# Performance work log

Hardware: AMD Instinct MI355X
Metric: run time of the kernel (lower is better)

The kernel has to match this reference:

```python
import jax, jax.numpy as jnp
import numpy as np

K_CLS, M_PROTO, C = 19, 10, 720
EPS_SK, SK_ITERS = 0.05, 3  # standard distributed_sinkhorn defaults (SwAV/ProtoSeg)


def _layernorm(x, g, b, eps=1e-5):
    mu = jnp.mean(x, axis=-1, keepdims=True)
    var = jnp.var(x, axis=-1, keepdims=True)
    return (x - mu) * jax.lax.rsqrt(var + eps) * g + b


def _l2n(x):
    return x / jnp.clip(jnp.linalg.norm(x, axis=-1, keepdims=True), 1e-12, None)


def _masked_sinkhorn(scores, mask):
    # scores: [K, N, M] per-class similarity; mask: [K, N] (1.0 where gt_seg == class k)
    # Faithful to distributed_sinkhorn(init_q) run per class, vectorized over classes
    # with masking instead of data-dependent boolean gather (jit-safe).
    L = jnp.exp(scores / EPS_SK) * mask[..., None]                     # [K, N, M]
    L = L / jnp.clip(jnp.sum(L, axis=(1, 2), keepdims=True), 1e-12, None)
    n = jnp.sum(mask, axis=1)[:, None, None]                           # pixels per class [K,1,1]
    n_safe = jnp.maximum(n, 1.0)

    def body(L, _):
        # normalize each prototype row (sum over pixels), then divide by M
        L = L / jnp.clip(jnp.sum(L, axis=1, keepdims=True), 1e-12, None) / M_PROTO
        # normalize each pixel column (sum over prototypes), then divide by n
        L = L / jnp.clip(jnp.sum(L, axis=2, keepdims=True), 1e-12, None) / n_safe
        L = L * mask[..., None]
        return L, None

    L, _ = jax.lax.scan(body, L, None, length=SK_ITERS)
    return L * n_safe                                                  # [K, N, M]


def setup_inputs() -> dict:
    key = jax.random.key(0)
    k1, k2, k3 = jax.random.split(key, 3)
    N = 4 * 128 * 128  # batch 4, 512x512 crop at HRNet output stride 4
    return {
        "x": jax.random.normal(k1, (N, C), jnp.float32),
        "gt_seg": jax.random.randint(k2, (N,), 0, K_CLS),
        "feat_gamma": jnp.ones((C,), jnp.float32),
        "feat_beta": jnp.zeros((C,), jnp.float32),
        "prototypes": jax.random.normal(k3, (K_CLS, M_PROTO, C), jnp.float32) * 0.02,
    }


def reference(x, gt_seg, feat_gamma, feat_beta, prototypes):
    # similarity_compute (cosine branch)
    xn = _l2n(_layernorm(x, feat_gamma, feat_beta))                    # [N, C]
    protos = _l2n(prototypes)                                          # [K, M, C]
    sim_mat = jnp.einsum('nd,kmd->nmk', xn, protos)                    # [N, M, K]

    # prototype_learning
    s = jnp.max(sim_mat, axis=1)                                       # amax over prototypes -> [N, K]
    pred_seg = jnp.argmax(s, axis=-1)                                  # [N]
    scores = jnp.transpose(sim_mat, (2, 0, 1))                         # [K, N, M]
    mask = jnp.transpose(jax.nn.one_hot(gt_seg, K_CLS, dtype=sim_mat.dtype))  # [K, N]
    q = _masked_sinkhorn(scores, mask)                                 # [K, N, M]
    return sim_mat, q, pred_seg
```

## Files before the change

### kernel.cpp

```cpp
#include <hip/hip_runtime.h>
#include <stdint.h>

#define N_PIX    65536
#define C_DIM    720
#define K_CLS    19
#define M_PROTO  10
#define NPROTO   190
#define CPAD     768
#define OFF_Q    12451840
#define OFF_PRED 24903680

typedef _Float16 half8 __attribute__((ext_vector_type(8)));
typedef _Float16 h4    __attribute__((ext_vector_type(4)));
typedef float    f32x4 __attribute__((ext_vector_type(4)));

#define WS_E       0u
#define WS_G2      768u
#define WS_G3      1536u
#define WS_CNT     2304u
#define WS_TIECNT  2432u
#define WS_PSCALE  4096u
#define WS_EPIX    1052672u
#define WS_U       3674112u
#define WS_TIELIST 3936256u
#define WS_PF16    4198400u
#define WS_PF32    4493312u

__device__ __forceinline__ void async16(const void* g, void* l) {
    __builtin_amdgcn_global_load_lds(
        (const __attribute__((address_space(1))) unsigned int*)g,
        (__attribute__((address_space(3))) unsigned int*)l, 16, 0, 0);
}

__global__ void proto_prep(const float* __restrict__ protos,
                           _Float16* __restrict__ pf16,
                           float* __restrict__ pf32,
                           float* __restrict__ wsf) {
    int p = blockIdx.x;
    int tid = threadIdx.x;
    if (p >= NPROTO) {
        for (int c = tid; c < CPAD; c += 256) pf16[(size_t)p * CPAD + c] = (_Float16)0.f;
        if (p == 191) for (int i = tid; i < 640; i += 256) wsf[i] = 0.f;
        return;
    }
    __shared__ float red[256];
    const float* row = protos + (size_t)p * C_DIM;
    float ss = 0.f;
    for (int c = tid; c < C_DIM; c += 256) { float v = row[c]; ss += v * v; }
    red[tid] = ss;
    __syncthreads();
    for (int s = 128; s > 0; s >>= 1) {
        if (tid < s) red[tid] += red[tid + s];
        __syncthreads();
    }
    float invn = 1.f / fmaxf(sqrtf(red[0]), 1e-12f);
    int e8 = p & 7;
    for (int c = tid; c < CPAD; c += 256) {
        float v = (c < C_DIM) ? row[c] * invn : 0.f;
        int sw = (((c >> 3) ^ e8) << 3) | (c & 7);
        pf16[(size_t)p * CPAD + sw] = (_Float16)v;
        if (c < C_DIM) pf32[(size_t)p * C_DIM + c] = v;
    }
}

__global__ __launch_bounds__(256) void gemm_fused(
        const float*  __restrict__ x,
        const float*  __restrict__ gamma,
        const float*  __restrict__ beta,
        const _Float16* __restrict__ pf16,
        const int*    __restrict__ gt_seg,
        float4* __restrict__ pscale,
        float* __restrict__ out_sim,
        float* __restrict__ out_pred,
        float* __restrict__ epix,
        float* __restrict__ E,
        float* __restrict__ cnt,
        int*   __restrict__ tiecnt,
        int*   __restrict__ tielist) {
    extern __shared__ __align__(16) char smem[];
    _Float16* xt = (_Float16*)smem;
    _Float16* ps = (_Float16*)(smem + 49152);

    int tid = threadIdx.x;
    int wave = tid >> 6, lane = tid & 63;
    int lane15 = lane & 15, quad = lane >> 4;
    int n0 = blockIdx.x * 32;
    int ph = wave & 1, qh = wave >> 1;
    int rsub = lane >> 3, csub = (lane & 7) << 3;

    const float4* g4 = (const float4*)gamma;
    const float4* b4 = (const float4*)beta;
    float4 gv[3], bv[3];
    #pragma unroll
    for (int j = 0; j < 3; ++j) {
        int f = lane + 64 * j;
        float4 z = make_float4(0.f, 0.f, 0.f, 0.f);
        gv[j] = (f < 180) ? g4[f] : z;
        bv[j] = (f < 180) ? b4[f] : z;
    }
    #pragma unroll 1
    for (int rr = 0; rr < 8; ++rr) {
        int row = wave * 8 + rr;
        int n = n0 + row;
        const float4* row4 = (const float4*)(x + (size_t)n * C_DIM);
        float a[8];
        #pragma unroll
        for (int t = 0; t < 8; ++t) a[t] = 0.f;
        float4 xv[3];
        #pragma unroll
        for (int j = 0; j < 3; ++j) {
            int f = lane + 64 * j;
            float4 z = make_float4(0.f, 0.f, 0.f, 0.f);
            float4 xvv = (f < 180) ? row4[f] : z;
            xv[j] = xvv;
            float4 gvv = gv[j], bvv = bv[j];
            #define ACC1(v, g, b) { float g2 = (g)*(g); a[0] += (v); a[1] += (v)*(v); \
                a[2] += (v)*g2; a[3] += (v)*(v)*g2; a[4] += (v)*(g)*(b); a[5] += g2; \
                a[6] += (g)*(b); a[7] += (b)*(b); }
            ACC1(xvv.x, gvv.x, bvv.x); ACC1(xvv.y, gvv.y, bvv.y);
            ACC1(xvv.z, gvv.z, bvv.z); ACC1(xvv.w, gvv.w, bvv.w);
            #undef ACC1
        }
        #pragma unroll
        for (int m = 1; m < 64; m <<= 1) {
            #pragma unroll
            for (int t = 0; t < 8; ++t) a[t] += __shfl_xor(a[t], m);
        }
        float mu   = a[0] * (1.f / 720.f);
        float var  = a[1] * (1.f / 720.f) - mu * mu;
        float rsig = rsqrtf(var + 1e-5f);
        float ny2  = rsig * rsig * (a[3] - 2.f * mu * a[2] + mu * mu * a[5])
                   + 2.f * rsig * (a[4] - mu * a[6]) + a[7];
        float rn   = 1.f / fmaxf(sqrtf(fmaxf(ny2, 0.f)), 1e-12f);
        float pp   = rsig * rn;
        float qq   = -pp * mu;
        if (lane == 0) pscale[n] = make_float4(pp, qq, rn, 0.f);
        #pragma unroll
        for (int j = 0; j < 3; ++j) {
            int f = lane + 64 * j;
            float4 xvv = xv[j], gvv = gv[j], bvv = bv[j];
            h4 o;
            o.x = (_Float16)((pp * xvv.x + qq) * gvv.x + rn * bvv.x);
            o.y = (_Float16)((pp * xvv.y + qq) * gvv.y + rn * bvv.y);
            o.z = (_Float16)((pp * xvv.z + qq) * gvv.z + rn * bvv.z);
            o.w = (_Float16)((pp * xvv.w + qq) * gvv.w + rn * bvv.w);
            int gl = f >> 1;
            int gp = (gl & 0x78) | ((gl ^ row) & 7);
            *reinterpret_cast<h4*>(xt + row * 768 + gp * 8 + (f & 1) * 4) = o;
        }
    }

    f32x4 acc[6];
    #pragma unroll
    for (int ct = 0; ct < 6; ++ct) acc[ct] = (f32x4){0.f, 0.f, 0.f, 0.f};

    int e8 = lane15 & 7;
    #pragma unroll 1
    for (int ch = 0; ch < 12; ++ch) {
        __syncthreads();
        #pragma unroll
        for (int i = 0; i < 6; ++i) {
            int r0 = wave * 48 + i * 8;
            const _Float16* g = pf16 + (size_t)(r0 + rsub) * CPAD + ch * 64 + csub;
            async16(g, ps + r0 * 64);
        }
        __syncthreads();
        #pragma unroll
        for (int ks = 0; ks < 2; ++ks) {
            int s = (ks * 4 + quad) ^ e8;
            half8 a0 = *reinterpret_cast<const half8*>(
                xt + (ph * 16 + lane15) * 768 + (ch * 8 + s) * 8);
            half8 b[6];
            #pragma unroll
            for (int ct = 0; ct < 6; ++ct)
                b[ct] = *reinterpret_cast<const half8*>(
                    ps + (qh * 96 + ct * 16 + lane15) * 64 + s * 8);
            #pragma unroll
            for (int ct = 0; ct < 6; ++ct)
                acc[ct] = __builtin_amdgcn_mfma_f32_16x16x32_f16(a0, b[ct], acc[ct], 0, 0, 0);
        }
    }

    __syncthreads();
    float* fsm   = (float*)smem;
    float* ebuf  = fsm;
    float* smaxs = fsm + 6400;
    float* Eks   = fsm + 7008;
    float* hist  = fsm + 7200;
    if (tid < 224) fsm[7008 + tid] = 0.f;
    #pragma unroll
    for (int ct = 0; ct < 6; ++ct) {
        int proto = qh * 96 + ct * 16 + lane15;
        if (proto < NPROTO) {
            int kc = proto / 10;
            int m = proto - kc * 10;
            int ob = m * 19 + kc;
            int prow = ph * 16 + quad * 4;
            #pragma unroll
            for (int r = 0; r < 4; ++r)
                ebuf[(prow + r) * 200 + ob] = acc[ct][r];
        }
    }
    __syncthreads();
    for (int t2 = tid; t2 < 32 * 192; t2 += 256) {
        int p = t2 / 192, col = t2 - p * 192;
        if (col < NPROTO)
            out_sim[(size_t)(n0 + p) * 190 + col] = ebuf[p * 200 + col];
    }
    for (int t2 = tid; t2 < 608; t2 += 256) {
        int p = t2 / 19, k = t2 - p * 19;
        const float* rowp = ebuf + p * 200;
        float mx = rowp[k];
        #pragma unroll
        for (int m = 1; m < 10; ++m) mx = fmaxf(mx, rowp[m * 19 + k]);
        smaxs[t2] = mx;
    }
    __syncthreads();
    if (tid < 32) {
        int p = tid;
        int pixel = n0 + p;
        float best = smaxs[p * 19], second = -1e30f;
        int bk = 0;
        #pragma unroll
        for (int k = 1; k < 19; ++k) {
            float v = smaxs[p * 19 + k];
            if (v > best) { second = best; best = v; bk = k; }
            else if (v > second) second = v;
        }
        out_pred[pixel] = (float)bk;
        if (best - second < 3e-4f) {
            int pos = atomicAdd(tiecnt, 1);
            if (pos < N_PIX) tielist[pos] = pixel;
        }
        int g = gt_seg[pixel];
        atomicAdd(&hist[g], 1.f);
        const float* rowp = ebuf + p * 200;
        #pragma unroll
        for (int m = 0; m < 10; ++m) {
            float ev = __expf(rowp[m * 19 + g] * 20.f);
            epix[(size_t)pixel * 10 + m] = ev;
            atomicAdd(&Eks[g * 10 + m], ev);
        }
    }
    __syncthreads();
    if (tid < 190) atomicAdd(&E[tid], Eks[tid]);
    if (tid < 19)  atomicAdd(&cnt[tid], hist[tid]);
}

__global__ void tiefix(const float* __restrict__ x,
                       const float4* __restrict__ pscale,
                       const float* __restrict__ gamma,
                       const float* __restrict__ beta,
                       const float* __restrict__ pf32,
                       const int* __restrict__ tiecnt,
                       const int* __restrict__ tielist,
                       float* __restrict__ out_pred) {
    __shared__ float xrow[720];
    __shared__ double sd[190];
    int count = *tiecnt;
    if (count > N_PIX) count = N_PIX;
    int wave = threadIdx.x >> 6, lane = threadIdx.x & 63;
    for (int it = blockIdx.x; it < count; it += gridDim.x) {
        int n = tielist[it];
        float4 sc = pscale[n];
        for (int c = threadIdx.x; c < 720; c += 256)
            xrow[c] = (sc.x * x[(size_t)n * 720 + c] + sc.y) * gamma[c] + sc.z * beta[c];
        __syncthreads();
        for (int p = wave; p < NPROTO; p += 4) {
            const float* pr = pf32 + (size_t)p * 720;
            double a = 0.0;
            for (int j = 0; j < 12; ++j) {
                int i = lane + 64 * j;
                if (i < 720) a += (double)xrow[i] * (double)pr[i];
            }
            #pragma unroll
            for (int m = 1; m < 64; m <<= 1) a += __shfl_xor(a, m);
            if (lane == 0) sd[p] = a;
        }
        __syncthreads();
        if (threadIdx.x == 0) {
            double best = -1e300;
            int bk = 0;
            for (int k = 0; k < 19; ++k) {
                double sk = -1e300;
                for (int m = 0; m < 10; ++m) sk = fmax(sk, sd[k * 10 + m]);
                if (sk > best) { best = sk; bk = k; }
            }
            out_pred[n] = (float)bk;
        }
        __syncthreads();
    }
}

__global__ void pk_fused(const float* __restrict__ epix,
                         const int* __restrict__ gt_seg,
                         const float* __restrict__ E,
                         const float* __restrict__ Gprev,
                         const float* __restrict__ cnt,
                         const float* __restrict__ uin,
                         float* __restrict__ uout,
                         float* __restrict__ Gout) {
    __shared__ float Es[190];
    __shared__ float vs[190];
    __shared__ float cs[19];
    __shared__ float Ga[190];
    int tid = threadIdx.x;
    if (tid < 190) { Es[tid] = E[tid]; Ga[tid] = 0.f; }
    if (tid < 19) cs[tid] = cnt[tid];
    __syncthreads();
    if (tid < 190) {
        int k = tid / 10;
        float S = 0.f;
        #pragma unroll
        for (int m = 0; m < 10; ++m) S += Es[k * 10 + m];
        float v0 = 1.f / fmaxf(S, 1e-12f);
        float vv = v0 / (fmaxf(v0 * Es[tid], 1e-12f) * 10.f);
        if (Gprev) vv = vv / (fmaxf(vv * Gprev[tid], 1e-12f) * 10.f);
        vs[tid] = vv;
    }
    __syncthreads();
    int n = blockIdx.x * 256 + tid;
    int g = gt_seg[n];
    float ns = fmaxf(cs[g], 1.f);
    const float* e = epix + (size_t)n * 10;
    float ev[10];
    float dot = 0.f;
    #pragma unroll
    for (int m = 0; m < 10; ++m) { ev[m] = e[m]; dot += ev[m] * vs[g * 10 + m]; }
    float up = uin ? uin[n] : 1.f;
    float c = up * dot;
    float uu = up / (fmaxf(c, 1e-12f) * ns);
    uout[n] = uu;
    #pragma unroll
    for (int m = 0; m < 10; ++m) atomicAdd(&Ga[g * 10 + m], ev[m] * uu);
    __syncthreads();
    if (tid < 190) atomicAdd(&Gout[tid], Ga[tid]);
}

__global__ void p3k_fused(const float* __restrict__ epix,
                          const int* __restrict__ gt_seg,
                          const float* __restrict__ E,
                          const float* __restrict__ G2,
                          const float* __restrict__ G3,
                          const float* __restrict__ cnt,
                          const float* __restrict__ uin,
                          float* __restrict__ qout) {
    __shared__ float Es[190];
    __shared__ float vs[190];
    __shared__ float cs[19];
    int tid = threadIdx.x;
    if (tid < 190) Es[tid] = E[tid];
    if (tid < 19) cs[tid] = cnt[tid];
    __syncthreads();
    if (tid < 190) {
        int k = tid / 10;
        float S = 0.f;
        #pragma unroll
        for (int m = 0; m < 10; ++m) S += Es[k * 10 + m];
        float v0 = 1.f / fmaxf(S, 1e-12f);
        float vv = v0 / (fmaxf(v0 * Es[tid], 1e-12f) * 10.f);
        vv = vv / (fmaxf(vv * G2[tid], 1e-12f) * 10.f);
        vv = vv / (fmaxf(vv * G3[tid], 1e-12f) * 10.f);
        vs[tid] = vv;
    }
    __syncthreads();
    int n = blockIdx.x * 256 + tid;
    int g = gt_seg[n];
    float ns = fmaxf(cs[g], 1.f);
    const float* e = epix + (size_t)n * 10;
    float ev[10];
    float dot = 0.f;
    #pragma unroll
    for (int m = 0; m < 10; ++m) { ev[m] = e[m]; dot += ev[m] * vs[g * 10 + m]; }
    float up = uin[n];
    float c = up * dot;
    float u3 = up / (fmaxf(c, 1e-12f) * ns);
    float2 qv[5];
    #pragma unroll
    for (int j = 0; j < 5; ++j) {
        qv[j].x = ev[2 * j] * u3 * vs[g * 10 + 2 * j] * ns;
        qv[j].y = ev[2 * j + 1] * u3 * vs[g * 10 + 2 * j + 1] * ns;
    }
    const float2 z2 = make_float2(0.f, 0.f);
    for (int k = 0; k < 19; ++k) {
        float2* dst = reinterpret_cast<float2*>(qout + (size_t)k * 655360 + (size_t)n * 10);
        if (k == g) {
            #pragma unroll
            for (int j = 0; j < 5; ++j) dst[j] = qv[j];
        } else {
            #pragma unroll
            for (int j = 0; j < 5; ++j) dst[j] = z2;
        }
    }
}

extern "C" void kernel_launch(void* const* d_in, const int* in_sizes, int n_in,
                              void* d_out, int out_size, void* d_ws, size_t ws_size,
                              hipStream_t stream) {
    const float* x      = (const float*)d_in[0];
    const int*   gt     = (const int*)d_in[1];
    const float* gamma  = (const float*)d_in[2];
    const float* beta   = (const float*)d_in[3];
    const float* protos = (const float*)d_in[4];
    float* out = (float*)d_out;
    char* ws = (char*)d_ws;

    float*  E       = (float*)(ws + WS_E);
    float*  G2      = (float*)(ws + WS_G2);
    float*  G3      = (float*)(ws + WS_G3);
    float*  cnt     = (float*)(ws + WS_CNT);
    int*    tiecnt  = (int*)(ws + WS_TIECNT);
    float4* pscale  = (float4*)(ws + WS_PSCALE);
    float*  epix    = (float*)(ws + WS_EPIX);
    float*  u       = (float*)(ws + WS_U);
    int*    tielist = (int*)(ws + WS_TIELIST);
    _Float16* pf16  = (_Float16*)(ws + WS_PF16);
    float*  pf32    = (float*)(ws + WS_PF32);

    static bool attr_set = false;
    if (!attr_set) {
        hipFuncSetAttribute((const void*)gemm_fused,
                            hipFuncAttributeMaxDynamicSharedMemorySize, 73728);
        attr_set = true;
    }

    proto_prep<<<192, 256, 0, stream>>>(protos, pf16, pf32, (float*)ws);
    gemm_fused<<<2048, 256, 73728, stream>>>(x, gamma, beta, pf16, gt, pscale,
                                             out, out + OFF_PRED, epix, E, cnt,
                                             tiecnt, tielist);
    tiefix<<<1024, 256, 0, stream>>>(x, pscale, gamma, beta, pf32, tiecnt, tielist, out + OFF_PRED);
    pk_fused<<<256, 256, 0, stream>>>(epix, gt, E, nullptr, cnt, nullptr, u, G2);
    pk_fused<<<256, 256, 0, stream>>>(epix, gt, E, G2, cnt, u, u, G3);
    p3k_fused<<<256, 256, 0, stream>>>(epix, gt, E, G2, G3, cnt, u, out + OFF_Q);
}
```

Baseline: 491.0 us.

## Give each wave its own prototype slice to drop per-chunk block barriers

The GEMM loop now assigns each wave its own 48-prototype slice, which it stages into a private LDS region and multiplies against all 32 pixel rows. Per-wave waitcnts replace the two block-wide __syncthreads per K chunk. All eight x rows per wave are also loaded up front for memory-level parallelism, and launch bounds now request 2 blocks per CU. The cost is more live registers from the xv[8][3] array, which risks spills under the tighter register budget.

```diff
diff --git a/kernel.cpp b/kernel.cpp
--- a/kernel.cpp
+++ b/kernel.cpp
@@ -63,7 +63,7 @@
     }
 }
 
-__global__ __launch_bounds__(256) void gemm_fused(
+__global__ __launch_bounds__(256, 2) void gemm_fused(
         const float*  __restrict__ x,
         const float*  __restrict__ gamma,
         const float*  __restrict__ beta,
@@ -85,7 +85,6 @@
     int wave = tid >> 6, lane = tid & 63;
     int lane15 = lane & 15, quad = lane >> 4;
     int n0 = blockIdx.x * 32;
-    int ph = wave & 1, qh = wave >> 1;
     int rsub = lane >> 3, csub = (lane & 7) << 3;
 
     const float4* g4 = (const float4*)gamma;
@@ -98,22 +97,28 @@
         gv[j] = (f < 180) ? g4[f] : z;
         bv[j] = (f < 180) ? b4[f] : z;
     }
-    #pragma unroll 1
+    float4 xv[8][3];
+    #pragma unroll
+    for (int rr = 0; rr < 8; ++rr) {
+        int row = wave * 8 + rr;
+        const float4* row4 = (const float4*)(x + (size_t)(n0 + row) * C_DIM);
+        #pragma unroll
+        for (int j = 0; j < 3; ++j) {
+            int f = lane + 64 * j;
+            float4 z = make_float4(0.f, 0.f, 0.f, 0.f);
+            xv[rr][j] = (f < 180) ? row4[f] : z;
+        }
+    }
+    #pragma unroll
     for (int rr = 0; rr < 8; ++rr) {
         int row = wave * 8 + rr;
         int n = n0 + row;
-        const float4* row4 = (const float4*)(x + (size_t)n * C_DIM);
         float a[8];
         #pragma unroll
         for (int t = 0; t < 8; ++t) a[t] = 0.f;
-        float4 xv[3];
         #pragma unroll
         for (int j = 0; j < 3; ++j) {
-            int f = lane + 64 * j;
-            float4 z = make_float4(0.f, 0.f, 0.f, 0.f);
-            float4 xvv = (f < 180) ? row4[f] : z;
-            xv[j] = xvv;
-            float4 gvv = gv[j], bvv = bv[j];
+            float4 xvv = xv[rr][j], gvv = gv[j], bvv = bv[j];
             #define ACC1(v, g, b) { float g2 = (g)*(g); a[0] += (v); a[1] += (v)*(v); \
                 a[2] += (v)*g2; a[3] += (v)*(v)*g2; a[4] += (v)*(g)*(b); a[5] += g2; \
                 a[6] += (g)*(b); a[7] += (b)*(b); }
@@ -138,7 +143,7 @@
         #pragma unroll
         for (int j = 0; j < 3; ++j) {
             int f = lane + 64 * j;
-            float4 xvv = xv[j], gvv = gv[j], bvv = bv[j];
+            float4 xvv = xv[rr][j], gvv = gv[j], bvv = bv[j];
             h4 o;
             o.x = (_Float16)((pp * xvv.x + qq) * gvv.x + rn * bvv.x);
             o.y = (_Float16)((pp * xvv.y + qq) * gvv.y + rn * bvv.y);
@@ -149,36 +154,42 @@
             *reinterpret_cast<h4*>(xt + row * 768 + gp * 8 + (f & 1) * 4) = o;
         }
     }
-
-    f32x4 acc[6];
-    #pragma unroll
-    for (int ct = 0; ct < 6; ++ct) acc[ct] = (f32x4){0.f, 0.f, 0.f, 0.f};
+    __syncthreads();
+
+    _Float16* myps = ps + wave * (48 * 64);
+    f32x4 acc[2][3];
+    #pragma unroll
+    for (int pt = 0; pt < 2; ++pt)
+        #pragma unroll
+        for (int ct = 0; ct < 3; ++ct) acc[pt][ct] = (f32x4){0.f, 0.f, 0.f, 0.f};
 
     int e8 = lane15 & 7;
     #pragma unroll 1
     for (int ch = 0; ch < 12; ++ch) {
-        __syncthreads();
         #pragma unroll
         for (int i = 0; i < 6; ++i) {
-            int r0 = wave * 48 + i * 8;
-            const _Float16* g = pf16 + (size_t)(r0 + rsub) * CPAD + ch * 64 + csub;
-            async16(g, ps + r0 * 64);
-        }
-        __syncthreads();
+            const _Float16* g = pf16 + (size_t)(wave * 48 + i * 8 + rsub) * CPAD + ch * 64 + csub;
+            async16(g, myps + i * 8 * 64);
+        }
+        asm volatile("s_waitcnt vmcnt(0)" ::: "memory");
+        __builtin_amdgcn_sched_barrier(0);
         #pragma unroll
         for (int ks = 0; ks < 2; ++ks) {
             int s = (ks * 4 + quad) ^ e8;
-            half8 a0 = *reinterpret_cast<const half8*>(
-                xt + (ph * 16 + lane15) * 768 + (ch * 8 + s) * 8);
-            half8 b[6];
-            #pragma unroll
-            for (int ct = 0; ct < 6; ++ct)
-                b[ct] = *reinterpret_cast<const half8*>(
-                    ps + (qh * 96 + ct * 16 + lane15) * 64 + s * 8);
-            #pragma unroll
-            for (int ct = 0; ct < 6; ++ct)
-                acc[ct] = __builtin_amdgcn_mfma_f32_16x16x32_f16(a0, b[ct], acc[ct], 0, 0, 0);
-        }
+            half8 a0 = *reinterpret_cast<const half8*>(xt + (lane15) * 768 + (ch * 8 + s) * 8);
+            half8 a1 = *reinterpret_cast<const half8*>(xt + (16 + lane15) * 768 + (ch * 8 + s) * 8);
+            half8 b[3];
+            #pragma unroll
+            for (int ct = 0; ct < 3; ++ct)
+                b[ct] = *reinterpret_cast<const half8*>(myps + (ct * 16 + lane15) * 64 + s * 8);
+            #pragma unroll
+            for (int ct = 0; ct < 3; ++ct) {
+                acc[0][ct] = __builtin_amdgcn_mfma_f32_16x16x32_f16(a0, b[ct], acc[0][ct], 0, 0, 0);
+                acc[1][ct] = __builtin_amdgcn_mfma_f32_16x16x32_f16(a1, b[ct], acc[1][ct], 0, 0, 0);
+            }
+        }
+        asm volatile("s_waitcnt lgkmcnt(0)" ::: "memory");
+        __builtin_amdgcn_sched_barrier(0);
     }
 
     __syncthreads();
@@ -189,16 +200,19 @@
     float* hist  = fsm + 7200;
     if (tid < 224) fsm[7008 + tid] = 0.f;
     #pragma unroll
-    for (int ct = 0; ct < 6; ++ct) {
-        int proto = qh * 96 + ct * 16 + lane15;
-        if (proto < NPROTO) {
-            int kc = proto / 10;
-            int m = proto - kc * 10;
-            int ob = m * 19 + kc;
-            int prow = ph * 16 + quad * 4;
-            #pragma unroll
-            for (int r = 0; r < 4; ++r)
-                ebuf[(prow + r) * 200 + ob] = acc[ct][r];
+    for (int pt = 0; pt < 2; ++pt) {
+        #pragma unroll
+        for (int ct = 0; ct < 3; ++ct) {
+            int proto = wave * 48 + ct * 16 + lane15;
+            if (proto < NPROTO) {
+                int kc = proto / 10;
+                int m = proto - kc * 10;
+                int ob = m * 19 + kc;
+                int prow = pt * 16 + quad * 4;
+                #pragma unroll
+                for (int r = 0; r < 4; ++r)
+                    ebuf[(prow + r) * 200 + ob] = acc[pt][ct][r];
+            }
         }
     }
     __syncthreads();
```

New measurement: 483.1 us. Within noise of the previous version (-1.6%).
